# Optimization experiments

Hardware: AMD Instinct MI355X
Metric: run time of the kernel (lower is better)

## Reference

```python
import jax, jax.numpy as jnp
import numpy as np

H = 256    # hidden_size
NH = 8     # num_heads
B = 256    # batch_size (num graphs)
M = 128    # max_num_nodes per graph
N = B * M  # total nodes
E = N * 16 # total edges


def _bn(x, g, b, eps=1e-5):
    # BatchNorm1d in training mode: batch stats over node dim, biased variance
    m = x.mean(0)
    v = ((x - m) ** 2).mean(0)
    return g * (x - m) * jax.lax.rsqrt(v + eps) + b


def setup_inputs() -> dict:
    key = jax.random.key(0)
    ks = jax.random.split(key, 12)
    def lin(k, o, i):
        return jax.random.normal(k, (o, i), jnp.float32) / np.sqrt(i).astype(np.float32)
    return {
        "h": jax.random.normal(ks[0], (N, H), jnp.float32),
        "gin_w1": lin(ks[1], H, H), "gin_b1": jnp.zeros((H,), jnp.float32),
        "gin_w2": lin(ks[2], H, H), "gin_b2": jnp.zeros((H,), jnp.float32),
        "in_proj_w": lin(ks[3], 3 * H, H), "in_proj_b": jnp.zeros((3 * H,), jnp.float32),
        "out_proj_w": lin(ks[4], H, H), "out_proj_b": jnp.zeros((H,), jnp.float32),
        "bn_local_g": jnp.ones((H,), jnp.float32), "bn_local_b": jnp.zeros((H,), jnp.float32),
        "bn_attn_g": jnp.ones((H,), jnp.float32), "bn_attn_b": jnp.zeros((H,), jnp.float32),
        "bn_out_g": jnp.ones((H,), jnp.float32), "bn_out_b": jnp.zeros((H,), jnp.float32),
        "ffn1_w": lin(ks[5], 2 * H, H), "ffn1_b": jnp.zeros((2 * H,), jnp.float32),
        "ffn2_w": lin(ks[6], H, 2 * H), "ffn2_b": jnp.zeros((H,), jnp.float32),
        "edge_src": jax.random.randint(ks[7], (E,), 0, N, dtype=jnp.int32),
        "edge_dst": jax.random.randint(ks[8], (E,), 0, N, dtype=jnp.int32),
        "batch_num_nodes": jnp.full((B,), M, dtype=jnp.int32),
    }


def reference(h, gin_w1, gin_b1, gin_w2, gin_b2, in_proj_w, in_proj_b,
              out_proj_w, out_proj_b, bn_local_g, bn_local_b, bn_attn_g, bn_attn_b,
              bn_out_g, bn_out_b, ffn1_w, ffn1_b, ffn2_w, ffn2_b,
              edge_src, edge_dst, batch_num_nodes):
    # ---- local GIN conv: gin_nn((1+eps)*h + sum_neighbors h), eps=0 ----
    agg = jax.ops.segment_sum(h[edge_src], edge_dst, num_segments=N)
    z = h + agg
    z = jax.nn.relu(z @ gin_w1.T + gin_b1) @ gin_w2.T + gin_b2
    h_local = _bn(h + z, bn_local_g, bn_local_b)  # dropout=0

    # ---- to_dense_batch scatter indices ----
    cum = jnp.concatenate([jnp.zeros((1,), batch_num_nodes.dtype), jnp.cumsum(batch_num_nodes)])
    node = jnp.arange(N, dtype=jnp.int32)
    bid = jnp.searchsorted(cum[1:], node, side='right')  # graph id per node
    idx = node - cum[bid] + bid * M                      # slot in dense [B*M]
    hd = jnp.zeros((B * M, H), h.dtype).at[idx].set(h).reshape(B, M, H)
    mask = jnp.zeros((B * M,), bool).at[idx].set(True).reshape(B, M)

    # ---- MultiheadAttention (batch_first, self-attn, key_padding_mask) ----
    qkv = hd @ in_proj_w.T + in_proj_b
    q, k, v = jnp.split(qkv, 3, axis=-1)
    dh = H // NH
    q = q.reshape(B, M, NH, dh)
    k = k.reshape(B, M, NH, dh)
    v = v.reshape(B, M, NH, dh)
    scores = jnp.einsum('bqhd,bkhd->bhqk', q, k) / np.float32(np.sqrt(dh))
    scores = jnp.where(mask[:, None, None, :], scores, jnp.float32(-1e9))
    attn = jax.nn.softmax(scores, axis=-1)
    ao = jnp.einsum('bhqk,bkhd->bqhd', attn, v).reshape(B, M, H)
    ao = ao @ out_proj_w.T + out_proj_b
    h_attn = ao.reshape(B * M, H)[idx]  # ragged gather back (x[mask])
    h_attn = _bn(h + h_attn, bn_attn_g, bn_attn_b)

    # ---- combine + FFN + out norm ----
    hh = h_local + h_attn
    hh = hh + (jax.nn.relu(hh @ ffn1_w.T + ffn1_b) @ ffn2_w.T + ffn2_b)
    return _bn(hh, bn_out_g, bn_out_b)
```

## Files before the change

### kernel.cpp

```cpp
#include <hip/hip_runtime.h>

#define NNODES 32768
#define HDIM   256
#define NHEADS 8
#define NB     256
#define NEDGES 524288


typedef unsigned short u16;
typedef unsigned int   u32;
typedef unsigned long long u64;
typedef __attribute__((ext_vector_type(8))) short short8;
typedef __attribute__((ext_vector_type(4))) float f32x4;

__device__ __forceinline__ float bf2f(u16 u){
  union { u32 i; float f; } x; x.i = ((u32)u) << 16; return x.f;
}
__device__ __forceinline__ u16 f2bf(float f){
  union { float f; u32 i; } x; x.f = f;
  u32 r = x.i + 0x7fffu + ((x.i >> 16) & 1u);
  return (u16)(r >> 16);
}
__device__ __forceinline__ void unpack8(uint4 v, float* f){
  f[0] = bf2f((u16)(v.x & 0xffff)); f[1] = bf2f((u16)(v.x >> 16));
  f[2] = bf2f((u16)(v.y & 0xffff)); f[3] = bf2f((u16)(v.y >> 16));
  f[4] = bf2f((u16)(v.z & 0xffff)); f[5] = bf2f((u16)(v.z >> 16));
  f[6] = bf2f((u16)(v.w & 0xffff)); f[7] = bf2f((u16)(v.w >> 16));
}
__device__ __forceinline__ uint4 pack8(const float* f){
  uint4 v;
  v.x = (u32)f2bf(f[0]) | ((u32)f2bf(f[1]) << 16);
  v.y = (u32)f2bf(f[2]) | ((u32)f2bf(f[3]) << 16);
  v.z = (u32)f2bf(f[4]) | ((u32)f2bf(f[5]) << 16);
  v.w = (u32)f2bf(f[6]) | ((u32)f2bf(f[7]) << 16);
  return v;
}

typedef __attribute__((address_space(3))) unsigned int lds_u32;
typedef const __attribute__((address_space(1))) unsigned int gbl_u32;
__device__ __forceinline__ void gload16(const void* g, void* l){
  __builtin_amdgcn_global_load_lds((gbl_u32*)(u64)g,
                                   (lds_u32*)(u32)(u64)l, 16, 0, 0);
}

struct CvtPtrs { const void* p[19]; };

__device__ static const int CVT_CH[19] = {
  2097152,16384,64,16384,64,49152,192,16384,64,64,64,64,64,64,64,32768,128,32768,64};
__device__ static const int CVT_PR[19] = {
  0,8388608,8454144,8454400,8519936,8520192,8716800,8717568,8783104,
  8783360,8783616,8783872,8784128,8784384,8784640,8784896,8915968,8916480,9047552};
#define CVT_TOTAL_CHUNKS 2261952

__global__ __launch_bounds__(256) void convert_k(CvtPtrs cp, u16* __restrict__ dst,
    const int* __restrict__ edge_dst, int* __restrict__ counts){
  int gid = blockIdx.x * 256 + threadIdx.x;
  if (gid < NEDGES) atomicAdd(&counts[edge_dst[gid]], 1);
  if (gid >= CVT_TOTAL_CHUNKS) return;
  int t = 0, rem = gid;
  while (t < 18 && rem >= CVT_CH[t]) { rem -= CVT_CH[t]; t++; }
  u16* d = dst + CVT_PR[t] + (size_t)rem * 4;
  float4 v = ((const float4*)cp.p[t])[rem];
  u16 o[4] = { f2bf(v.x), f2bf(v.y), f2bf(v.z), f2bf(v.w) };
  *(uint2*)d = *(const uint2*)o;
}

__global__ void scan_k(const int* __restrict__ counts, int* __restrict__ offsets,
                       int* __restrict__ cursor, float* __restrict__ stats){
  __shared__ int part[1024];
  int t = threadIdx.x;
  stats[t] = 0.0f;
  if (t < 512) stats[1024 + t] = 0.0f;
  int local[32];
  int s = 0;
  int base = t * 32;
#pragma unroll
  for (int i = 0; i < 32; i++){ local[i] = counts[base + i]; s += local[i]; }
  part[t] = s;
  __syncthreads();
  for (int off = 1; off < 1024; off <<= 1){
    int v = (t >= off) ? part[t - off] : 0;
    __syncthreads();
    part[t] += v;
    __syncthreads();
  }
  int run = part[t] - s;
#pragma unroll
  for (int i = 0; i < 32; i++){
    offsets[base + i] = run; cursor[base + i] = run; run += local[i];
  }
  if (t == 1023) offsets[NNODES] = run;
}

__global__ void bucket_k(const int* __restrict__ src, const int* __restrict__ dst,
                         int* __restrict__ cursor, int* __restrict__ srcs){
  int e = blockIdx.x * 256 + threadIdx.x;
  int p = atomicAdd(&cursor[dst[e]], 1);
  srcs[p] = src[e];
}

__global__ __launch_bounds__(256) void agg_k(const u16* __restrict__ h,
    const int* __restrict__ offsets, const int* __restrict__ srcs,
    u16* __restrict__ z0){
  int node = blockIdx.x * 4 + (threadIdx.x >> 6);
  int lane = threadIdx.x & 63;
  size_t coff = (size_t)lane * 4;
  int beg = offsets[node], end = offsets[node + 1];

  uint2 self = *(const uint2*)&h[(size_t)node * HDIM + coff];
  float a0 = bf2f((u16)(self.x & 0xffff)), a1 = bf2f((u16)(self.x >> 16));
  float a2 = bf2f((u16)(self.y & 0xffff)), a3 = bf2f((u16)(self.y >> 16));

  int e = beg;
  for (; e + 8 <= end; e += 8){
    uint2 v[8];
#pragma unroll
    for (int i = 0; i < 8; i++){
      int s = srcs[e + i];
      v[i] = *(const uint2*)&h[(size_t)s * HDIM + coff];
    }
#pragma unroll
    for (int i = 0; i < 8; i++){
      a0 += bf2f((u16)(v[i].x & 0xffff));
      a1 += bf2f((u16)(v[i].x >> 16));
      a2 += bf2f((u16)(v[i].y & 0xffff));
      a3 += bf2f((u16)(v[i].y >> 16));
    }
  }
  for (; e < end; e++){
    int s = srcs[e];
    uint2 va = *(const uint2*)&h[(size_t)s * HDIM + coff];
    a0 += bf2f((u16)(va.x & 0xffff));
    a1 += bf2f((u16)(va.x >> 16));
    a2 += bf2f((u16)(va.y & 0xffff));
    a3 += bf2f((u16)(va.y >> 16));
  }

  uint2 o;
  o.x = (u32)f2bf(a0) | ((u32)f2bf(a1) << 16);
  o.y = (u32)f2bf(a2) | ((u32)f2bf(a3) << 16);
  *(uint2*)&z0[(size_t)node * HDIM + coff] = o;
}

__device__ __forceinline__ void mfma_step(const u16* AS_, const u16* WS_,
    f32x4 (&acc)[4][4], int wm, int wn, int ln, int qs){
  short8 af[4], bfr[4];
#pragma unroll
  for (int mt = 0; mt < 4; mt++)
    af[mt] = *(const short8*)&AS_[(wm * 64 + mt * 16 + ln) * 32 + qs];
#pragma unroll
  for (int nt = 0; nt < 4; nt++)
    bfr[nt] = *(const short8*)&WS_[(wn * 64 + nt * 16 + ln) * 32 + qs];
#pragma unroll
  for (int mt = 0; mt < 4; mt++)
#pragma unroll
    for (int nt = 0; nt < 4; nt++)
      acc[mt][nt] = __builtin_amdgcn_mfma_f32_16x16x32_bf16(af[mt], bfr[nt], acc[mt][nt], 0, 0, 0);
}

template<int K>
__device__ __forceinline__ void kloop(const u16* __restrict__ A,
    const u16* __restrict__ W, u16* smem, int m0, int n0, int tid,
    f32x4 (&acc)[4][4]){
  u16* As0 = smem;        u16* Ws0 = smem + 4096;
  u16* As1 = smem + 8192; u16* Ws1 = smem + 12288;
  const int wave = tid >> 6, lane = tid & 63;
  const int wm = wave >> 1, wn = wave & 1;
  const int ln = lane & 15, q4 = lane >> 4;
  const int qs = (q4 ^ ((ln >> 1) & 3)) << 3;
  const int r_l = tid >> 2;
  const int csw = ((tid & 3) ^ ((tid >> 3) & 3)) << 3;
  const u16* gA = A + (size_t)(m0 + r_l) * K + csw;
  const u16* gW = W + (size_t)(n0 + r_l) * K + csw;
  u16* dA0 = As0 + wave * 512; u16* dW0 = Ws0 + wave * 512;
  u16* dA1 = As1 + wave * 512; u16* dW1 = Ws1 + wave * 512;
  const int NT = K / 32;

  gload16(gA, dA0); gload16(gA + 64 * K, dA0 + 2048);
  gload16(gW, dW0); gload16(gW + 64 * K, dW0 + 2048);
  __syncthreads();

#pragma unroll
  for (int t = 0; t < NT; t += 2){
    if (t + 1 < NT){
      int kn = (t + 1) * 32;
      gload16(gA + kn, dA1); gload16(gA + 64 * K + kn, dA1 + 2048);
      gload16(gW + kn, dW1); gload16(gW + 64 * K + kn, dW1 + 2048);
    }
    mfma_step(As0, Ws0, acc, wm, wn, ln, qs);
    __syncthreads();
    if (t + 2 < NT){
      int kn = (t + 2) * 32;
      gload16(gA + kn, dA0); gload16(gA + 64 * K + kn, dA0 + 2048);
      gload16(gW + kn, dW0); gload16(gW + 64 * K + kn, dW0 + 2048);
    }
    mfma_step(As1, Ws1, acc, wm, wn, ln, qs);
    __syncthreads();
  }
}

struct GemmCfg {
  const u16* A; const u16* W; const u16* bias; const u16* res;
  u16* C; float* ssum; float* ssq;
  int NO; int nx; int relu;
};

__device__ __forceinline__ void remap(int f, int nx, int& m0, int& n0){
  int xcd = f & 7, j = f >> 3;
  m0 = (xcd + ((j / nx) << 3)) << 7;
  n0 = (j % nx) << 7;
}

template<bool RES, bool STATS>
__device__ __forceinline__ void epilogue(f32x4 (&acc)[4][4], u16* smem,
    const GemmCfg& c, int m0, int n0, int tid){
  const int NO = c.NO;
  const int wave = tid >> 6, lane = tid & 63;
  const int wm = wave >> 1, wn = wave & 1;
  const int q4 = lane >> 4, ln = lane & 15;

  if (RES){
#pragma unroll
    for (int i = 0; i < 8; i++){
      int ch = tid + i * 256;
      int r = ch >> 4, k = ch & 15;
      uint4 vv = *(const uint4*)&c.res[(size_t)(m0 + r) * NO + n0 + (k << 3)];
      *(uint4*)&smem[r * 128 + ((((k >> 1) ^ (r & 7)) << 4)) + ((k & 1) << 3)] = vv;
    }
    __syncthreads();
  }

#pragma unroll
  for (int nt = 0; nt < 4; nt++){
    int lcol = wn * 64 + nt * 16 + ln;
    int gcol = n0 + lcol;
    float bv = bf2f(c.bias[gcol]);
    int chunk = lcol >> 4;
    float cs = 0.0f, cq = 0.0f;
#pragma unroll
    for (int mt = 0; mt < 4; mt++){
      int lrow = wm * 64 + mt * 16 + q4 * 4;
#pragma unroll
      for (int reg = 0; reg < 4; reg++){
        int r = lrow + reg;
        int sidx = r * 128 + ((chunk ^ (r & 7)) << 4) + ln;
        float v = acc[mt][nt][reg] + bv;
        if (c.relu) v = fmaxf(v, 0.0f);
        if (RES) v += bf2f(smem[sidx]);
        smem[sidx] = f2bf(v);
        if (STATS){ cs += v; cq += v * v; }
      }
    }
    if (STATS){
      cs += __shfl_xor(cs, 16); cs += __shfl_xor(cs, 32);
      cq += __shfl_xor(cq, 16); cq += __shfl_xor(cq, 32);
      if (lane < 16){
        atomicAdd(&c.ssum[gcol], cs);
        atomicAdd(&c.ssq[gcol], cq);
      }
    }
  }
  __syncthreads();

#pragma unroll
  for (int i = 0; i < 8; i++){
    int ch = tid + i * 256;
    int r = ch >> 4, k = ch & 15;
    uint4 vv = *(const uint4*)&smem[r * 128 + (((k >> 1) ^ (r & 7)) << 4) + ((k & 1) << 3)];
    *(uint4*)&c.C[(size_t)(m0 + r) * NO + n0 + (k << 3)] = vv;
  }
}

template<int K, bool RES, bool STATS>
__global__ __launch_bounds__(256) void gemm_one(GemmCfg c){
  __shared__ u16 smem[16384];
  const int tid = threadIdx.x;
  int m0, n0; remap(blockIdx.x, c.nx, m0, n0);
  f32x4 acc[4][4] = {};
  kloop<K>(c.A, c.W, smem, m0, n0, tid, acc);
  epilogue<RES, STATS>(acc, smem, c, m0, n0, tid);
}

__global__ __launch_bounds__(256) void gemm_dual(GemmCfg c0, GemmCfg c1, int split){
  __shared__ u16 smem[16384];
  const int tid = threadIdx.x;
  const int fid = blockIdx.x;
  GemmCfg c = (fid < split) ? c0 : c1;
  int f = (fid < split) ? fid : fid - split;
  int m0, n0; remap(f, c.nx, m0, n0);
  f32x4 acc[4][4] = {};
  kloop<256>(c.A, c.W, smem, m0, n0, tid, acc);
  epilogue<false, false>(acc, smem, c, m0, n0, tid);
}

__global__ __launch_bounds__(256) void attn_k(const u16* __restrict__ qkv,
                                              u16* __restrict__ ao){
  __shared__ u16 Qs[128 * 40];
  __shared__ u16 Ks[128 * 40];
  __shared__ u16 VTs[32 * 136];
  __shared__ u16 Ps[128 * 136];

  const int b  = blockIdx.x >> 3;
  const int nh = blockIdx.x & 7;
  const int tid = threadIdx.x;
  const int wave = tid >> 6, lane = tid & 63;
  const int q4 = lane >> 4, ln = lane & 15;

#pragma unroll
  for (int c2 = 0; c2 < 2; c2++){
    int chunk = tid + c2 * 256;
    int r = chunk >> 2;
    int cc = chunk & 3;
    size_t nb = (size_t)(b * 128 + r) * 768 + nh * 32 + cc * 8;
    uint4 vq = *(const uint4*)&qkv[nb];
    uint4 vk = *(const uint4*)&qkv[nb + 256];
    uint4 vv = *(const uint4*)&qkv[nb + 512];
    *(uint4*)&Qs[r * 40 + cc * 8] = vq;
    *(uint4*)&Ks[r * 40 + cc * 8] = vk;
    union { uint4 v; u16 h[8]; } uv; uv.v = vv;
#pragma unroll
    for (int i = 0; i < 8; i++) VTs[(cc * 8 + i) * 136 + r] = uv.h[i];
  }
  __syncthreads();

  f32x4 accs[2][8] = {};
  short8 qf[2];
#pragma unroll
  for (int mt = 0; mt < 2; mt++)
    qf[mt] = *(const short8*)&Qs[(wave * 32 + mt * 16 + ln) * 40 + q4 * 8];
#pragma unroll
  for (int nt = 0; nt < 8; nt++){
    short8 kf = *(const short8*)&Ks[(nt * 16 + ln) * 40 + q4 * 8];
    accs[0][nt] = __builtin_amdgcn_mfma_f32_16x16x32_bf16(qf[0], kf, accs[0][nt], 0, 0, 0);
    accs[1][nt] = __builtin_amdgcn_mfma_f32_16x16x32_bf16(qf[1], kf, accs[1][nt], 0, 0, 0);
  }

  const float scale = 0.17677669529663687f;
  float invs[2][4];
#pragma unroll
  for (int mt = 0; mt < 2; mt++){
#pragma unroll
    for (int reg = 0; reg < 4; reg++){
      float rm = -1e30f;
#pragma unroll
      for (int nt = 0; nt < 8; nt++){
        accs[mt][nt][reg] *= scale;
        rm = fmaxf(rm, accs[mt][nt][reg]);
      }
      for (int m = 1; m < 16; m <<= 1) rm = fmaxf(rm, __shfl_xor(rm, m));
      float rs = 0.0f;
#pragma unroll
      for (int nt = 0; nt < 8; nt++){
        float e = __expf(accs[mt][nt][reg] - rm);
        accs[mt][nt][reg] = e;
        rs += e;
      }
      for (int m = 1; m < 16; m <<= 1) rs += __shfl_xor(rs, m);
      invs[mt][reg] = 1.0f / rs;
    }
  }

#pragma unroll
  for (int mt = 0; mt < 2; mt++)
#pragma unroll
    for (int nt = 0; nt < 8; nt++)
#pragma unroll
      for (int reg = 0; reg < 4; reg++)
        Ps[(wave * 32 + mt * 16 + q4 * 4 + reg) * 136 + nt * 16 + ln] =
            f2bf(accs[mt][nt][reg] * invs[mt][reg]);
  __syncthreads();

  f32x4 acco[2][2] = {};
#pragma unroll
  for (int kk = 0; kk < 4; kk++){
    short8 pf[2], vf[2];
#pragma unroll
    for (int mt = 0; mt < 2; mt++)
      pf[mt] = *(const short8*)&Ps[(wave * 32 + mt * 16 + ln) * 136 + kk * 32 + q4 * 8];
#pragma unroll
    for (int nt = 0; nt < 2; nt++)
      vf[nt] = *(const short8*)&VTs[(nt * 16 + ln) * 136 + kk * 32 + q4 * 8];
#pragma unroll
    for (int mt = 0; mt < 2; mt++)
#pragma unroll
      for (int nt = 0; nt < 2; nt++)
        acco[mt][nt] = __builtin_amdgcn_mfma_f32_16x16x32_bf16(pf[mt], vf[nt], acco[mt][nt], 0, 0, 0);
  }

  __syncthreads();
  u16* Os = Ps;
#pragma unroll
  for (int mt = 0; mt < 2; mt++)
#pragma unroll
    for (int nt = 0; nt < 2; nt++)
#pragma unroll
      for (int reg = 0; reg < 4; reg++)
        Os[(wave * 32 + mt * 16 + q4 * 4 + reg) * 40 + nt * 16 + ln] =
            f2bf(acco[mt][nt][reg]);
  __syncthreads();
#pragma unroll
  for (int i = 0; i < 2; i++){
    int ch = tid + i * 256;
    int r = ch >> 2, k = ch & 3;
    uint4 vv = *(const uint4*)&Os[r * 40 + k * 8];
    *(uint4*)&ao[(size_t)(b * 128 + r) * HDIM + nh * 32 + k * 8] = vv;
  }
}

__global__ __launch_bounds__(256) void combine_k(const u16* __restrict__ xl,
    const u16* __restrict__ xa, const float* __restrict__ stats,
    const u16* __restrict__ gl, const u16* __restrict__ bl,
    const u16* __restrict__ ga, const u16* __restrict__ ba,
    u16* __restrict__ hh){
  __shared__ float cs0[256], cs1[256], cs2[256];
  int t = threadIdx.x;
  {
    const float invN = 1.0f / 32768.0f;
    float mA = stats[t] * invN;
    float vA = stats[256 + t] * invN - mA * mA;
    float sA = bf2f(gl[t]) * rsqrtf(vA + 1e-5f);
    float tA = bf2f(bl[t]) - mA * sA;
    float mB = stats[512 + t] * invN;
    float vB = stats[768 + t] * invN - mB * mB;
    float sB = bf2f(ga[t]) * rsqrtf(vB + 1e-5f);
    float tB = bf2f(ba[t]) - mB * sB;
    cs0[t] = sA; cs1[t] = sB; cs2[t] = tA + tB;
  }
  __syncthreads();
  int gid = blockIdx.x * 256 + t;
  size_t off = (size_t)gid * 8;
  int cb = (int)(off & 255);
  float sl[8], sa[8], tt[8];
  *(float4*)&sl[0] = *(const float4*)&cs0[cb];
  *(float4*)&sl[4] = *(const float4*)&cs0[cb + 4];
  *(float4*)&sa[0] = *(const float4*)&cs1[cb];
  *(float4*)&sa[4] = *(const float4*)&cs1[cb + 4];
  *(float4*)&tt[0] = *(const float4*)&cs2[cb];
  *(float4*)&tt[4] = *(const float4*)&cs2[cb + 4];
  float fl[8], fa[8], fo[8];
  unpack8(*(const uint4*)&xl[off], fl);
  unpack8(*(const uint4*)&xa[off], fa);
#pragma unroll
  for (int i = 0; i < 8; i++) fo[i] = sl[i] * fl[i] + sa[i] * fa[i] + tt[i];
  *(uint4*)&hh[off] = pack8(fo);
}

__global__ __launch_bounds__(256) void finalbn_k(const u16* __restrict__ y,
    const float* __restrict__ stats, const u16* __restrict__ g,
    const u16* __restrict__ bb, float* __restrict__ out){
  __shared__ float cs0[256], cs1[256];
  int t = threadIdx.x;
  {
    const float invN = 1.0f / 32768.0f;
    float m = stats[1024 + t] * invN;
    float v = stats[1280 + t] * invN - m * m;
    float s = bf2f(g[t]) * rsqrtf(v + 1e-5f);
    cs0[t] = s; cs1[t] = bf2f(bb[t]) - m * s;
  }
  __syncthreads();
  int gid = blockIdx.x * 256 + t;
  size_t off = (size_t)gid * 8;
  int cb = (int)(off & 255);
  float ss[8], tt[8];
  *(float4*)&ss[0] = *(const float4*)&cs0[cb];
  *(float4*)&ss[4] = *(const float4*)&cs0[cb + 4];
  *(float4*)&tt[0] = *(const float4*)&cs1[cb];
  *(float4*)&tt[4] = *(const float4*)&cs1[cb + 4];
  float fy[8], fo[8];
  unpack8(*(const uint4*)&y[off], fy);
#pragma unroll
  for (int i = 0; i < 8; i++) fo[i] = ss[i] * fy[i] + tt[i];
  *(float4*)&out[off] = *(const float4*)&fo[0];
  *(float4*)&out[off + 4] = *(const float4*)&fo[4];
}

extern "C" void kernel_launch(void* const* d_in, const int* in_sizes, int n_in,
                              void* d_out, int out_size, void* d_ws, size_t ws_size,
                              hipStream_t stream){
  const int* edge_src = (const int*)d_in[19];
  const int* edge_dst = (const int*)d_in[20];

  char* ws = (char*)d_ws;
  float* stats = (float*)ws;
  u16*   conv  = (u16*)(ws + 12288);
  u16*   A     = (u16*)(ws + 12288 + 18095616);
  u16*   Bb    = (u16*)(ws + 12288 + 18095616 + 16777216);
  u16*   C     = (u16*)d_out;
  const size_t BIG_NEED = 51662336ull + 50331648ull;
  const bool big = (ws_size >= BIG_NEED);
  u16* QKV = (u16*)(ws + 51662336);

  int* counts  = (int*)Bb;
  int* offsets = (int*)((char*)Bb + 131072);
  int* cursor  = (int*)((char*)Bb + 262400);
  int* srcs    = (int*)((char*)Bb + 393472);

  const u16* convH = conv;
  const u16* W1  = conv + 8388608; const u16* b1g = conv + 8454144;
  const u16* W2  = conv + 8454400; const u16* b2g = conv + 8519936;
  const u16* Win = conv + 8520192; const u16* bin = conv + 8716800;
  const u16* Wo  = conv + 8717568; const u16* bo  = conv + 8783104;
  const u16* g_l = conv + 8783360; const u16* b_l = conv + 8783616;
  const u16* g_a = conv + 8783872; const u16* b_a = conv + 8784128;
  const u16* g_o = conv + 8784384; const u16* b_o = conv + 8784640;
  const u16* Wf1 = conv + 8784896; const u16* bf1 = conv + 8915968;
  const u16* Wf2 = conv + 8916480; const u16* bf2 = conv + 9047552;

  hipMemsetAsync(counts, 0, 131072, stream);

  CvtPtrs cp;
  for (int i = 0; i < 19; i++) cp.p[i] = d_in[i];
  convert_k<<<8836, 256, 0, stream>>>(cp, conv, edge_dst, counts);

  scan_k<<<1, 1024, 0, stream>>>(counts, offsets, cursor, stats);
  bucket_k<<<NEDGES / 256, 256, 0, stream>>>(edge_src, edge_dst, cursor, srcs);
  agg_k<<<NNODES / 4, 256, 0, stream>>>(convH, offsets, srcs, A);

  if (big){
    GemmCfg cg1  = { A,     W1,  b1g, nullptr, Bb,  nullptr, nullptr, 256, 2, 1 };
    GemmCfg cqkv = { convH, Win, bin, nullptr, QKV, nullptr, nullptr, 768, 6, 0 };
    gemm_dual<<<512 + 1536, 256, 0, stream>>>(cg1, cqkv, 512);

    attn_k<<<2048, 256, 0, stream>>>(QKV, C);

    GemmCfg cg2 = { Bb, W2, b2g, convH, A, stats + 0, stats + 256, 256, 2, 0 };
    gemm_one<256, true, true><<<512, 256, 0, stream>>>(cg2);
  } else {
    GemmCfg cg1 = { A, W1, b1g, nullptr, Bb, nullptr, nullptr, 256, 2, 1 };
    gemm_one<256, false, false><<<512, 256, 0, stream>>>(cg1);
    GemmCfg cg2 = { Bb, W2, b2g, convH, A, stats + 0, stats + 256, 256, 2, 0 };
    gemm_one<256, true, true><<<512, 256, 0, stream>>>(cg2);
    for (int c = 0; c < 4; c++){
      const u16* hA = convH + (size_t)c * 8192 * HDIM;
      u16* aoC = C + (size_t)c * 8192 * HDIM;
      GemmCfg cq = { hA, Win, bin, nullptr, Bb, nullptr, nullptr, 768, 6, 0 };
      gemm_one<256, false, false><<<384, 256, 0, stream>>>(cq);
      attn_k<<<512, 256, 0, stream>>>(Bb, aoC);
    }
  }

  GemmCfg cop = { C, Wo, bo, convH, Bb, stats + 512, stats + 768, 256, 2, 0 };
  gemm_one<256, true, true><<<512, 256, 0, stream>>>(cop);

  combine_k<<<4096, 256, 0, stream>>>(A, Bb, stats, g_l, b_l, g_a, b_a, C);

  GemmCfg cf1 = { C, Wf1, bf1, nullptr, A, nullptr, nullptr, 512, 4, 1 };
  gemm_one<256, false, false><<<1024, 256, 0, stream>>>(cf1);
  GemmCfg cf2 = { A, Wf2, bf2, C, (u16*)conv, stats + 1024, stats + 1280, 256, 2, 0 };
  gemm_one<512, true, true><<<512, 256, 0, stream>>>(cf2);

  finalbn_k<<<4096, 256, 0, stream>>>(conv, stats, g_o, b_o, (float*)d_out);
}
```

Before: 405.9 us.

## Fuse QKV projection into attention kernel, drop QKV intermediate buffer

Each attention block (one graph, one head) now computes its own Q, K and V slice directly from h and the in-projection weights with MFMA, staged through shared memory, instead of reading a precomputed QKV tensor. The separate QKV GEMM, the dual-GEMM kernel, and the large-workspace branch are removed, so the QKV intermediate is no longer written to and read back from global memory. In exchange, h rows are re-read once per head (8x) and the GIN first GEMM no longer shares a launch with the QKV GEMM.

```diff
diff --git a/kernel.cpp b/kernel.cpp
--- a/kernel.cpp
+++ b/kernel.cpp
@@ -281,24 +281,15 @@
   epilogue<RES, STATS>(acc, smem, c, m0, n0, tid);
 }
 
-__global__ __launch_bounds__(256) void gemm_dual(GemmCfg c0, GemmCfg c1, int split){
-  __shared__ u16 smem[16384];
-  const int tid = threadIdx.x;
-  const int fid = blockIdx.x;
-  GemmCfg c = (fid < split) ? c0 : c1;
-  int f = (fid < split) ? fid : fid - split;
-  int m0, n0; remap(f, c.nx, m0, n0);
-  f32x4 acc[4][4] = {};
-  kloop<256>(c.A, c.W, smem, m0, n0, tid, acc);
-  epilogue<false, false>(acc, smem, c, m0, n0, tid);
-}
-
-__global__ __launch_bounds__(256) void attn_k(const u16* __restrict__ qkv,
-                                              u16* __restrict__ ao){
+__global__ __launch_bounds__(256) void attn_fused_k(const u16* __restrict__ h,
+    const u16* __restrict__ Win, const u16* __restrict__ bin,
+    u16* __restrict__ ao){
   __shared__ u16 Qs[128 * 40];
   __shared__ u16 Ks[128 * 40];
   __shared__ u16 VTs[32 * 136];
   __shared__ u16 Ps[128 * 136];
+  u16* As = Ps;
+  u16* Wsl = Ps + 9216;
 
   const int b  = blockIdx.x >> 3;
   const int nh = blockIdx.x & 7;
@@ -306,21 +297,79 @@
   const int wave = tid >> 6, lane = tid & 63;
   const int q4 = lane >> 4, ln = lane & 15;
 
-#pragma unroll
-  for (int c2 = 0; c2 < 2; c2++){
-    int chunk = tid + c2 * 256;
-    int r = chunk >> 2;
-    int cc = chunk & 3;
-    size_t nb = (size_t)(b * 128 + r) * 768 + nh * 32 + cc * 8;
-    uint4 vq = *(const uint4*)&qkv[nb];
-    uint4 vk = *(const uint4*)&qkv[nb + 256];
-    uint4 vv = *(const uint4*)&qkv[nb + 512];
-    *(uint4*)&Qs[r * 40 + cc * 8] = vq;
-    *(uint4*)&Ks[r * 40 + cc * 8] = vk;
-    union { uint4 v; u16 h[8]; } uv; uv.v = vv;
-#pragma unroll
-    for (int i = 0; i < 8; i++) VTs[(cc * 8 + i) * 136 + r] = uv.h[i];
-  }
+  f32x4 acc[2][6] = {};
+  uint4 ra[4], rw[3];
+  const int ac = (tid & 7) << 3;
+
+  auto loadqkv = [&](int k0){
+#pragma unroll
+    for (int i = 0; i < 4; i++){
+      int r = (tid + i * 256) >> 3;
+      ra[i] = *(const uint4*)&h[(size_t)(b * 128 + r) * 256 + k0 + ac];
+    }
+#pragma unroll
+    for (int i = 0; i < 3; i++){
+      int wc = tid + i * 256;
+      int wr = wc >> 3;
+      int gr = ((wr >> 5) << 8) + nh * 32 + (wr & 31);
+      rw[i] = *(const uint4*)&Win[(size_t)gr * 256 + k0 + ((wc & 7) << 3)];
+    }
+  };
+
+  loadqkv(0);
+#pragma unroll
+  for (int s = 0; s < 4; s++){
+    __syncthreads();
+#pragma unroll
+    for (int i = 0; i < 4; i++){
+      int r = (tid + i * 256) >> 3;
+      *(uint4*)&As[r * 72 + ac] = ra[i];
+    }
+#pragma unroll
+    for (int i = 0; i < 3; i++){
+      int wc = tid + i * 256;
+      *(uint4*)&Wsl[(wc >> 3) * 72 + ((wc & 7) << 3)] = rw[i];
+    }
+    if (s < 3) loadqkv((s + 1) * 64);
+    __syncthreads();
+#pragma unroll
+    for (int kk = 0; kk < 2; kk++){
+      short8 af[2], bf[6];
+#pragma unroll
+      for (int mt = 0; mt < 2; mt++)
+        af[mt] = *(const short8*)&As[(wave * 32 + mt * 16 + ln) * 72 + kk * 32 + q4 * 8];
+#pragma unroll
+      for (int nt = 0; nt < 6; nt++)
+        bf[nt] = *(const short8*)&Wsl[(nt * 16 + ln) * 72 + kk * 32 + q4 * 8];
+#pragma unroll
+      for (int mt = 0; mt < 2; mt++)
+#pragma unroll
+        for (int nt = 0; nt < 6; nt++)
+          acc[mt][nt] = __builtin_amdgcn_mfma_f32_16x16x32_bf16(af[mt], bf[nt], acc[mt][nt], 0, 0, 0);
+    }
+  }
+
+  float bv[6];
+#pragma unroll
+  for (int nt = 0; nt < 6; nt++){
+    int c96 = nt * 16 + ln;
+    bv[nt] = bf2f(bin[((c96 >> 5) << 8) + nh * 32 + (c96 & 31)]);
+  }
+#pragma unroll
+  for (int mt = 0; mt < 2; mt++)
+#pragma unroll
+    for (int nt = 0; nt < 6; nt++){
+      int c96 = nt * 16 + ln;
+      int g = c96 >> 5, c32 = c96 & 31;
+#pragma unroll
+      for (int reg = 0; reg < 4; reg++){
+        int row = wave * 32 + mt * 16 + q4 * 4 + reg;
+        u16 val = f2bf(acc[mt][nt][reg] + bv[nt]);
+        if (g == 0) Qs[row * 40 + c32] = val;
+        else if (g == 1) Ks[row * 40 + c32] = val;
+        else VTs[c32 * 136 + row] = val;
+      }
+    }
   __syncthreads();
 
   f32x4 accs[2][8] = {};
@@ -486,9 +535,6 @@
   u16*   A     = (u16*)(ws + 12288 + 18095616);
   u16*   Bb    = (u16*)(ws + 12288 + 18095616 + 16777216);
   u16*   C     = (u16*)d_out;
-  const size_t BIG_NEED = 51662336ull + 50331648ull;
-  const bool big = (ws_size >= BIG_NEED);
-  u16* QKV = (u16*)(ws + 51662336);
 
   int* counts  = (int*)Bb;
   int* offsets = (int*)((char*)Bb + 131072);
@@ -516,28 +562,12 @@
   bucket_k<<<NEDGES / 256, 256, 0, stream>>>(edge_src, edge_dst, cursor, srcs);
   agg_k<<<NNODES / 4, 256, 0, stream>>>(convH, offsets, srcs, A);
 
-  if (big){
-    GemmCfg cg1  = { A,     W1,  b1g, nullptr, Bb,  nullptr, nullptr, 256, 2, 1 };
-    GemmCfg cqkv = { convH, Win, bin, nullptr, QKV, nullptr, nullptr, 768, 6, 0 };
-    gemm_dual<<<512 + 1536, 256, 0, stream>>>(cg1, cqkv, 512);
-
-    attn_k<<<2048, 256, 0, stream>>>(QKV, C);
-
-    GemmCfg cg2 = { Bb, W2, b2g, convH, A, stats + 0, stats + 256, 256, 2, 0 };
-    gemm_one<256, true, true><<<512, 256, 0, stream>>>(cg2);
-  } else {
-    GemmCfg cg1 = { A, W1, b1g, nullptr, Bb, nullptr, nullptr, 256, 2, 1 };
-    gemm_one<256, false, false><<<512, 256, 0, stream>>>(cg1);
-    GemmCfg cg2 = { Bb, W2, b2g, convH, A, stats + 0, stats + 256, 256, 2, 0 };
-    gemm_one<256, true, true><<<512, 256, 0, stream>>>(cg2);
-    for (int c = 0; c < 4; c++){
-      const u16* hA = convH + (size_t)c * 8192 * HDIM;
-      u16* aoC = C + (size_t)c * 8192 * HDIM;
-      GemmCfg cq = { hA, Win, bin, nullptr, Bb, nullptr, nullptr, 768, 6, 0 };
-      gemm_one<256, false, false><<<384, 256, 0, stream>>>(cq);
-      attn_k<<<512, 256, 0, stream>>>(Bb, aoC);
-    }
-  }
+  attn_fused_k<<<2048, 256, 0, stream>>>(convH, Win, bin, C);
+
+  GemmCfg cg1 = { A, W1, b1g, nullptr, Bb, nullptr, nullptr, 256, 2, 1 };
+  gemm_one<256, false, false><<<512, 256, 0, stream>>>(cg1);
+  GemmCfg cg2 = { Bb, W2, b2g, convH, A, stats + 0, stats + 256, 256, 2, 0 };
+  gemm_one<256, true, true><<<512, 256, 0, stream>>>(cg2);
 
   GemmCfg cop = { C, Wo, bo, convH, Bb, stats + 512, stats + 768, 256, 2, 0 };
   gemm_one<256, true, true><<<512, 256, 0, stream>>>(cop);
```

Result: slower. 443.9 us (+9.3%).

## Triple-buffer GEMM K-loop with vmcnt waits and single barrier per step

Applied to the files above, without the earlier changes.

Replaces the double-buffered GEMM main loop with a three-stage LDS ring buffer. Loads are issued two tiles ahead, and the loop uses explicit s_waitcnt vmcnt with a single barrier per K step instead of two __syncthreads. The goal is to hide more global-load latency and cut barrier overhead. In exchange, the GEMM kernels need 48KB instead of 32KB of shared memory, which may lower occupancy.

```diff
diff --git a/kernel.cpp b/kernel.cpp
--- a/kernel.cpp
+++ b/kernel.cpp
@@ -162,8 +162,6 @@
 __device__ __forceinline__ void kloop(const u16* __restrict__ A,
     const u16* __restrict__ W, u16* smem, int m0, int n0, int tid,
     f32x4 (&acc)[4][4]){
-  u16* As0 = smem;        u16* Ws0 = smem + 4096;
-  u16* As1 = smem + 8192; u16* Ws1 = smem + 12288;
   const int wave = tid >> 6, lane = tid & 63;
   const int wm = wave >> 1, wn = wave & 1;
   const int ln = lane & 15, q4 = lane >> 4;
@@ -172,31 +170,30 @@
   const int csw = ((tid & 3) ^ ((tid >> 3) & 3)) << 3;
   const u16* gA = A + (size_t)(m0 + r_l) * K + csw;
   const u16* gW = W + (size_t)(n0 + r_l) * K + csw;
-  u16* dA0 = As0 + wave * 512; u16* dW0 = Ws0 + wave * 512;
-  u16* dA1 = As1 + wave * 512; u16* dW1 = Ws1 + wave * 512;
+  u16* dA = smem + wave * 512;
+  u16* dW = smem + 4096 + wave * 512;
   const int NT = K / 32;
 
-  gload16(gA, dA0); gload16(gA + 64 * K, dA0 + 2048);
-  gload16(gW, dW0); gload16(gW + 64 * K, dW0 + 2048);
-  __syncthreads();
-
-#pragma unroll
-  for (int t = 0; t < NT; t += 2){
-    if (t + 1 < NT){
-      int kn = (t + 1) * 32;
-      gload16(gA + kn, dA1); gload16(gA + 64 * K + kn, dA1 + 2048);
-      gload16(gW + kn, dW1); gload16(gW + 64 * K + kn, dW1 + 2048);
-    }
-    mfma_step(As0, Ws0, acc, wm, wn, ln, qs);
-    __syncthreads();
-    if (t + 2 < NT){
-      int kn = (t + 2) * 32;
-      gload16(gA + kn, dA0); gload16(gA + 64 * K + kn, dA0 + 2048);
-      gload16(gW + kn, dW0); gload16(gW + 64 * K + kn, dW0 + 2048);
-    }
-    mfma_step(As1, Ws1, acc, wm, wn, ln, qs);
-    __syncthreads();
-  }
+#define STAGE(bb, kt) do { const int kn = (kt) * 32;                      \
+    u16* pa = dA + (bb) * 8192; u16* pw = dW + (bb) * 8192;               \
+    gload16(gA + kn, pa); gload16(gA + 64 * K + kn, pa + 2048);           \
+    gload16(gW + kn, pw); gload16(gW + 64 * K + kn, pw + 2048); } while(0)
+
+  STAGE(0, 0);
+  STAGE(1, 1);
+#pragma unroll
+  for (int t = 0; t < NT; t++){
+    if (t + 1 < NT) asm volatile("s_waitcnt vmcnt(4)" ::: "memory");
+    else            asm volatile("s_waitcnt vmcnt(0)" ::: "memory");
+    __builtin_amdgcn_s_barrier();
+    __builtin_amdgcn_sched_barrier(0);
+    if (t + 2 < NT) STAGE((t + 2) % 3, t + 2);
+    const u16* bse = smem + (t % 3) * 8192;
+    mfma_step(bse, bse + 4096, acc, wm, wn, ln, qs);
+    __builtin_amdgcn_sched_barrier(0);
+  }
+#undef STAGE
+  __syncthreads();
 }
 
 struct GemmCfg {
@@ -273,7 +270,7 @@
 
 template<int K, bool RES, bool STATS>
 __global__ __launch_bounds__(256) void gemm_one(GemmCfg c){
-  __shared__ u16 smem[16384];
+  __shared__ u16 smem[24576];
   const int tid = threadIdx.x;
   int m0, n0; remap(blockIdx.x, c.nx, m0, n0);
   f32x4 acc[4][4] = {};
@@ -282,7 +279,7 @@
 }
 
 __global__ __launch_bounds__(256) void gemm_dual(GemmCfg c0, GemmCfg c1, int split){
-  __shared__ u16 smem[16384];
+  __shared__ u16 smem[24576];
   const int tid = threadIdx.x;
   const int fid = blockIdx.x;
   GemmCfg c = (fid < split) ? c0 : c1;
```

After: 401.6 us. About the same (-1.1%).
